# Optimization experiments

Measured on AMD Instinct MI355X. Metric: run time of the kernel, lower is better.

## Reference

```python
import jax, jax.numpy as jnp
import numpy as np

D_IN, D_ATTN, STEPS = 1024, 64, 2
P_TOP, TAU, LN_EPS = 0.9, 1.0, 1e-5
N = 4096

def _xavier(key, shape):
    fan_in, fan_out = shape[0], shape[1]
    lim = jnp.sqrt(6.0 / (fan_in + fan_out))
    return jax.random.uniform(key, shape, jnp.float32, -lim, lim)

def setup_inputs() -> dict:
    key = jax.random.key(0)
    ks = jax.random.split(key, 12)
    X = jax.random.normal(ks[0], (N, D_IN), jnp.float32)
    S = jax.random.uniform(ks[1], (N, N), jnp.float32)
    # weights stored so that y = x @ W (transposed vs torch nn.Linear.weight)
    W1 = _xavier(ks[2], (D_IN, D_ATTN))
    W3 = _xavier(ks[3], (D_IN, D_ATTN))
    W2 = _xavier(ks[4], (D_ATTN, D_ATTN))  # used raw: Q @ W2 @ K.T
    U1_0 = _xavier(ks[5], (D_IN, D_IN))
    U1_1 = _xavier(ks[6], (D_IN, D_IN))
    U2_0 = _xavier(ks[7], (D_IN, D_IN))
    U2_1 = _xavier(ks[8], (D_IN, D_IN))
    gamma = jnp.ones((D_IN,), jnp.float32)
    beta = jnp.zeros((D_IN,), jnp.float32)
    return {"X": X, "S": S, "W1": W1, "W2": W2, "W3": W3,
            "U1_0": U1_0, "U1_1": U1_1, "U2_0": U2_0, "U2_1": U2_1,
            "gamma": gamma, "beta": beta}

def _adj_from_feats(Xa, W1, W2, W3):
    # bilinear attention logits: (N, N)
    Q = Xa @ W1
    K = Xa @ W3
    logits = (Q @ W2) @ K.T / TAU
    n = logits.shape[1]
    order = jnp.argsort(-logits, axis=1)                       # descending
    vals = jnp.take_along_axis(logits, order, axis=1)
    probs = jax.nn.softmax(vals, axis=1)
    csum = jnp.cumsum(probs, axis=1)
    k_i = jnp.sum(csum < P_TOP, axis=1) + 1                    # per-row top-p count
    keep = jnp.arange(n)[None, :] < k_i[:, None]
    masked_sorted = jnp.where(keep, vals, -jnp.inf)
    rows = jnp.arange(n)[:, None]
    masked = jnp.full_like(logits, -jnp.inf).at[rows, order].set(masked_sorted)
    return jax.nn.softmax(masked, axis=1)

def reference(X, S, W1, W2, W3, U1_0, U1_1, U2_0, U2_1, gamma, beta):
    n = X.shape[0]
    S = S + jnp.eye(n, dtype=X.dtype)
    R = S / jnp.clip(S.sum(axis=1, keepdims=True), 1e-12)      # row-normalized prior
    Z = jnp.zeros_like(X)
    Xf, Xa = X, X
    U1s, U2s = (U1_0, U1_1), (U2_0, U2_1)
    for s in range(STEPS):
        A = _adj_from_feats(Xa, W1, W2, W3)
        Xf = R @ Xf
        Xa = A @ Xa
        Z = Z + (Xf @ U1s[s] + Xa @ U2s[s])                    # dropout = identity (eval)
    Y = X + Z
    mu = Y.mean(axis=-1, keepdims=True)
    var = Y.var(axis=-1, keepdims=True)
    return (Y - mu) * jax.lax.rsqrt(var + LN_EPS) * gamma + beta
```

## Files before the change

kernel.cpp:

```cpp
#include <hip/hip_runtime.h>
#include <cstddef>
#include <cmath>

#define N_TOK 4096
#define D_INF 1024
#define OB_Q 384

typedef unsigned long long u64;
typedef __attribute__((ext_vector_type(8))) short bf16x8;
typedef __attribute__((ext_vector_type(4))) float f32x4;

__device__ __forceinline__ float blockSum(float x, float* red) {
#pragma unroll
  for (int o = 32; o; o >>= 1) x += __shfl_xor(x, o);
  __syncthreads();
  if ((threadIdx.x & 63) == 0) red[threadIdx.x >> 6] = x;
  __syncthreads();
  return (red[0] + red[1]) + (red[2] + red[3]);
}

__device__ __forceinline__ int blockSumI512(int x, int* red) {
#pragma unroll
  for (int o = 32; o; o >>= 1) x += __shfl_xor(x, o);
  __syncthreads();
  if ((threadIdx.x & 63) == 0) red[threadIdx.x >> 6] = x;
  __syncthreads();
  int s = 0;
#pragma unroll
  for (int w = 0; w < 8; ++w) s += red[w];
  return s;
}

__device__ __forceinline__ float np_expf(float x) {
  const float log2e = 1.44269504088896341f;
  float q = __builtin_rintf(x * log2e);
  float r = __builtin_fmaf(q, -0.693359375f, x);
  r = __builtin_fmaf(q, 2.12194440e-4f, r);
  float poly = 1.9875691500e-4f;
  poly = __builtin_fmaf(poly, r, 1.3981999507e-3f);
  poly = __builtin_fmaf(poly, r, 8.3334519073e-3f);
  poly = __builtin_fmaf(poly, r, 4.1665795894e-2f);
  poly = __builtin_fmaf(poly, r, 1.6666665459e-1f);
  poly = __builtin_fmaf(poly, r, 5.0000001201e-1f);
  float zz = r * r;
  poly = __builtin_fmaf(poly, zz, r);
  poly = poly + 1.0f;
  return __builtin_ldexpf(poly, (int)q);
}

__device__ __forceinline__ int PIDX(int i) {
  return (i & ~127) | ((i + (i >> 7)) & 127);
}

__device__ float npPairwiseSum4096Rot(const float* __restrict__ buf, float* share) {
  int t = threadIdx.x;
  __syncthreads();
  if (t < 32) {
    const float* a = buf + (t << 7);
    float r0 = a[t & 127], r1 = a[(t + 1) & 127], r2 = a[(t + 2) & 127],
          r3 = a[(t + 3) & 127];
    float r4 = a[(t + 4) & 127], r5 = a[(t + 5) & 127], r6 = a[(t + 6) & 127],
          r7 = a[(t + 7) & 127];
    for (int i = 8; i < 128; i += 8) {
      r0 += a[(i + 0 + t) & 127]; r1 += a[(i + 1 + t) & 127];
      r2 += a[(i + 2 + t) & 127]; r3 += a[(i + 3 + t) & 127];
      r4 += a[(i + 4 + t) & 127]; r5 += a[(i + 5 + t) & 127];
      r6 += a[(i + 6 + t) & 127]; r7 += a[(i + 7 + t) & 127];
    }
    float leaf = ((r0 + r1) + (r2 + r3)) + ((r4 + r5) + (r6 + r7));
    leaf += __shfl_xor(leaf, 1);
    leaf += __shfl_xor(leaf, 2);
    leaf += __shfl_xor(leaf, 4);
    leaf += __shfl_xor(leaf, 8);
    leaf += __shfl_xor(leaf, 16);
    if (t == 0) share[0] = leaf;
  }
  __syncthreads();
  return share[0];
}

__device__ __forceinline__ unsigned desc_key(float v) {
  unsigned u = __float_as_uint(v);
  unsigned m = (u & 0x80000000u) ? ~u : (u | 0x80000000u);
  return ~m;
}
__device__ __forceinline__ float desc_key_inv(unsigned k) {
  unsigned m = ~k;
  return __uint_as_float((m & 0x80000000u) ? (m ^ 0x80000000u) : ~m);
}

__device__ __forceinline__ u64 ballot_match8(int d) {
  u64 m = ~0ull;
#pragma unroll
  for (int b = 0; b < 8; ++b) {
    u64 bal = __ballot((d >> b) & 1);
    m &= ((d >> b) & 1) ? bal : ~bal;
  }
  return m;
}

__device__ __forceinline__ unsigned short f2bf(float f) {
  unsigned u = __float_as_uint(f);
  return (unsigned short)((u + 0x7FFFu + ((u >> 16) & 1u)) >> 16);
}

__global__ __launch_bounds__(256) void rowsum_kernel(const float* __restrict__ S,
                                                     float* __restrict__ rs) {
  __shared__ float red[4];
  const float* s = S + (size_t)blockIdx.x * N_TOK;
  float acc = 0.f;
  for (int j = threadIdx.x; j < N_TOK; j += 256) acc += s[j];
  acc = blockSum(acc, red);
  if (threadIdx.x == 0) rs[blockIdx.x] = 1.0f / fmaxf(acc + 1.0f, 1e-12f);
}

__global__ void wcat_kernel(const float* __restrict__ W1,
                            const float* __restrict__ W3, float* __restrict__ Wc) {
  int r = blockIdx.x;
  int c = threadIdx.x;
  Wc[r * 128 + c] = (c < 64) ? W1[r * 64 + c] : W3[r * 64 + (c - 64)];
}

__global__ __launch_bounds__(256) void qw_kernel(const float* __restrict__ QK,
                                                 const float* __restrict__ W2,
                                                 float* __restrict__ QW) {
  __shared__ float w[64][65];
  int t = threadIdx.x;
#pragma unroll
  for (int v = 0; v < 16; ++v) {
    int idx = t + v * 256;
    w[idx >> 6][idx & 63] = W2[idx];
  }
  __syncthreads();
  int row = blockIdx.x * 4 + (t >> 6);
  int c = t & 63;
  const float* q = QK + (size_t)row * 128;
  float acc = 0.f;
#pragma unroll
  for (int k = 0; k < 64; ++k) acc = __builtin_fmaf(q[k], w[k][c], acc);
  QW[(size_t)row * 64 + c] = acc;
}

__device__ __forceinline__ int ob_step(int rem) {
  if (rem >= 2 * OB_Q) return OB_Q;
  if (rem > OB_Q) return ((rem / 2) + 15) & ~15;
  return rem;
}

template <int BETA>
__global__ __launch_bounds__(256) void gemm_tile(const float* __restrict__ A,
                                                 const float* __restrict__ B,
                                                 float* __restrict__ C,
                                                 int M, int N, int K) {
  __shared__ float As[16][68];
  __shared__ float Bs[16][68];
  int t = threadIdx.x;
  int tx = t & 15, ty = t >> 4;
  int row0 = blockIdx.y * 64, col0 = blockIdx.x * 64;
  float tot[4][4] = {};
  float acc[4][4] = {};
  int next_b = ob_step(K);
  for (int k0 = 0; k0 < K; k0 += 16) {
    if (k0 == next_b) {
#pragma unroll
      for (int i = 0; i < 4; ++i)
#pragma unroll
        for (int j = 0; j < 4; ++j) { tot[i][j] += acc[i][j]; acc[i][j] = 0.f; }
      next_b = k0 + ob_step(K - k0);
    }
#pragma unroll
    for (int v = 0; v < 4; ++v) {
      int idx = t + v * 256;
      int r = idx >> 4, c = idx & 15;
      As[c][r] = A[(size_t)(row0 + r) * K + k0 + c];
    }
#pragma unroll
    for (int v = 0; v < 4; ++v) {
      int idx = t + v * 256;
      int r = idx >> 6, c = idx & 63;
      Bs[r][c] = B[(size_t)(k0 + r) * N + col0 + c];
    }
    __syncthreads();
#pragma unroll
    for (int kk = 0; kk < 16; ++kk) {
      float4 a = *(const float4*)&As[kk][ty * 4];
      float4 b = *(const float4*)&Bs[kk][tx * 4];
      float av[4] = {a.x, a.y, a.z, a.w};
      float bv[4] = {b.x, b.y, b.z, b.w};
#pragma unroll
      for (int i = 0; i < 4; ++i)
#pragma unroll
        for (int j = 0; j < 4; ++j)
          acc[i][j] = __builtin_fmaf(av[i], bv[j], acc[i][j]);
    }
    __syncthreads();
  }
#pragma unroll
  for (int i = 0; i < 4; ++i)
#pragma unroll
    for (int j = 0; j < 4; ++j) tot[i][j] += acc[i][j];
#pragma unroll
  for (int i = 0; i < 4; ++i) {
    float* cp = &C[(size_t)(row0 + ty * 4 + i) * N + col0 + tx * 4];
    float4 o;
    if (BETA) {
      float4 old = *(const float4*)cp;
      o.x = old.x + tot[i][0]; o.y = old.y + tot[i][1];
      o.z = old.z + tot[i][2]; o.w = old.w + tot[i][3];
    } else {
      o.x = tot[i][0]; o.y = tot[i][1]; o.z = tot[i][2]; o.w = tot[i][3];
    }
    *(float4*)cp = o;
  }
}

__global__ __launch_bounds__(256) void spmm_exact(const float* __restrict__ A,
                                                  const float* __restrict__ X,
                                                  float* __restrict__ C) {
  __shared__ unsigned short idxs[N_TOK];
  __shared__ int wq[4];
  int t = threadIdx.x;
  int lane = t & 63, w = t >> 6;
  int row = blockIdx.x;
  const float* a = A + (size_t)row * N_TOK;

  int base = t * 16;
  int c0 = 0;
#pragma unroll
  for (int u = 0; u < 16; ++u) c0 += (a[base + u] != 0.f) ? 1 : 0;
  int incl = c0;
#pragma unroll
  for (int d = 1; d < 64; d <<= 1) {
    int up = __shfl_up(incl, d);
    if (lane >= d) incl += up;
  }
  if (lane == 63) wq[w] = incl;
  __syncthreads();
  int off = 0;
  for (int ww = 0; ww < w; ++ww) off += wq[ww];
  int total = wq[0] + wq[1] + wq[2] + wq[3];
  int pos = off + incl - c0;
#pragma unroll
  for (int u = 0; u < 16; ++u)
    if (a[base + u] != 0.f) idxs[pos++] = (unsigned short)(base + u);
  __syncthreads();

  int c = t * 4;
  float acc0 = 0.f, acc1 = 0.f, acc2 = 0.f, acc3 = 0.f;
  float tt0 = 0.f, tt1 = 0.f, tt2 = 0.f, tt3 = 0.f;
  int nb = ob_step(N_TOK);
  for (int q = 0; q < total; ++q) {
    int j = idxs[q];
    while (j >= nb) {
      tt0 += acc0; tt1 += acc1; tt2 += acc2; tt3 += acc3;
      acc0 = acc1 = acc2 = acc3 = 0.f;
      nb += ob_step(N_TOK - nb);
    }
    float av = a[j];
    float4 xv = *(const float4*)&X[(size_t)j * D_INF + c];
    acc0 = __builtin_fmaf(av, xv.x, acc0);
    acc1 = __builtin_fmaf(av, xv.y, acc1);
    acc2 = __builtin_fmaf(av, xv.z, acc2);
    acc3 = __builtin_fmaf(av, xv.w, acc3);
  }
  tt0 += acc0; tt1 += acc1; tt2 += acc2; tt3 += acc3;
  float4 o = {tt0, tt1, tt2, tt3};
  *(float4*)&C[(size_t)row * D_INF + c] = o;
}

template <int BETA>
__global__ __launch_bounds__(256) void gemm_bf16(const float* __restrict__ A,
                                                 const float* __restrict__ B,
                                                 float* __restrict__ C,
                                                 int M, int N, int K) {
  __shared__ unsigned short As[128 * 32];
  __shared__ unsigned short Bs[128 * 32];
  const int t = threadIdx.x;
  const int l = t & 63, w = t >> 6, wr = w >> 1, wc = w & 1;
  const int m0 = blockIdx.y * 128, n0 = blockIdx.x * 128;

  f32x4 acc[4][4];
#pragma unroll
  for (int i = 0; i < 4; ++i)
#pragma unroll
    for (int j = 0; j < 4; ++j)
#pragma unroll
      for (int r = 0; r < 4; ++r) acc[i][j][r] = 0.f;

  const int argp = t >> 3;
  const int acc4 = (t & 7) * 4;
  const int bkb = t >> 5;
  const int bnb = t & 31;

  for (int k0 = 0; k0 < K; k0 += 32) {
#pragma unroll
    for (int u = 0; u < 4; ++u) {
      int row = argp * 4 + u;
      float4 v = *(const float4*)&A[(size_t)(m0 + row) * K + k0 + acc4];
      ushort4 h;
      h.x = f2bf(v.x); h.y = f2bf(v.y); h.z = f2bf(v.z); h.w = f2bf(v.w);
      int idx = (row * 32 + acc4) ^ (((row >> 1) & 3) << 3);
      *(ushort4*)&As[idx] = h;
    }
    {
      float4 r0 = *(const float4*)&B[(size_t)(k0 + bkb * 4 + 0) * N + n0 + bnb * 4];
      float4 r1 = *(const float4*)&B[(size_t)(k0 + bkb * 4 + 1) * N + n0 + bnb * 4];
      float4 r2 = *(const float4*)&B[(size_t)(k0 + bkb * 4 + 2) * N + n0 + bnb * 4];
      float4 r3 = *(const float4*)&B[(size_t)(k0 + bkb * 4 + 3) * N + n0 + bnb * 4];
      float c0[4] = {r0.x, r0.y, r0.z, r0.w};
      float c1[4] = {r1.x, r1.y, r1.z, r1.w};
      float c2[4] = {r2.x, r2.y, r2.z, r2.w};
      float c3[4] = {r3.x, r3.y, r3.z, r3.w};
#pragma unroll
      for (int u = 0; u < 4; ++u) {
        int nrow = bnb * 4 + u;
        ushort4 h;
        h.x = f2bf(c0[u]); h.y = f2bf(c1[u]); h.z = f2bf(c2[u]); h.w = f2bf(c3[u]);
        int idx = (nrow * 32 + bkb * 4) ^ (((nrow >> 1) & 3) << 3);
        *(ushort4*)&Bs[idx] = h;
      }
    }
    __syncthreads();
    bf16x8 af[4], bfv[4];
    const int kseg = (l >> 4) * 8;
#pragma unroll
    for (int fr = 0; fr < 4; ++fr) {
      int row = wr * 64 + fr * 16 + (l & 15);
      int idx = (row * 32 + kseg) ^ (((row >> 1) & 3) << 3);
      af[fr] = *(const bf16x8*)&As[idx];
    }
#pragma unroll
    for (int fc = 0; fc < 4; ++fc) {
      int nrow = wc * 64 + fc * 16 + (l & 15);
      int idx = (nrow * 32 + kseg) ^ (((nrow >> 1) & 3) << 3);
      bfv[fc] = *(const bf16x8*)&Bs[idx];
    }
#pragma unroll
    for (int fr = 0; fr < 4; ++fr)
#pragma unroll
      for (int fc = 0; fc < 4; ++fc)
        acc[fr][fc] = __builtin_amdgcn_mfma_f32_16x16x32_bf16(af[fr], bfv[fc],
                                                              acc[fr][fc], 0, 0, 0);
    __syncthreads();
  }
#pragma unroll
  for (int fr = 0; fr < 4; ++fr) {
#pragma unroll
    for (int fc = 0; fc < 4; ++fc) {
      int rbase = m0 + wr * 64 + fr * 16 + ((l >> 4) << 2);
      int col = n0 + wc * 64 + fc * 16 + (l & 15);
#pragma unroll
      for (int r = 0; r < 4; ++r) {
        size_t off = (size_t)(rbase + r) * N + col;
        float v = acc[fr][fc][r];
        C[off] = BETA ? (C[off] + v) : v;
      }
    }
  }
}

__global__ __launch_bounds__(256) void logits_abt(const float* __restrict__ QW,
                                                  const float* __restrict__ QK,
                                                  float* __restrict__ L) {
  __shared__ float Aq[64][68];
  __shared__ float Bk[64][68];
  int t = threadIdx.x;
  int tx = t & 15, ty = t >> 4;
  int row0 = blockIdx.y * 64, col0 = blockIdx.x * 64;
#pragma unroll
  for (int v = 0; v < 16; ++v) {
    int idx = t + v * 256;
    int c = idx & 63, r = idx >> 6;
    Aq[c][r] = QW[(size_t)(row0 + r) * 64 + c];
    Bk[c][r] = QK[(size_t)(col0 + r) * 128 + 64 + c];
  }
  __syncthreads();
  float acc[4][4] = {};
#pragma unroll
  for (int c0 = 0; c0 < 64; ++c0) {
    float4 a = *(const float4*)&Aq[c0][ty * 4];
    float4 b = *(const float4*)&Bk[c0][tx * 4];
    float av[4] = {a.x, a.y, a.z, a.w};
    float bv[4] = {b.x, b.y, b.z, b.w};
#pragma unroll
    for (int i = 0; i < 4; ++i)
#pragma unroll
      for (int j = 0; j < 4; ++j)
        acc[i][j] = __builtin_fmaf(av[i], bv[j], acc[i][j]);
  }
#pragma unroll
  for (int i = 0; i < 4; ++i) {
    float4 o = {acc[i][0], acc[i][1], acc[i][2], acc[i][3]};
    *(float4*)&L[(size_t)(row0 + ty * 4 + i) * N_TOK + col0 + tx * 4] = o;
  }
}

__global__ __launch_bounds__(512, 6) void topp_exact(float* __restrict__ L) {
  __shared__ unsigned key[N_TOK];
  __shared__ unsigned scr[N_TOK];
  __shared__ unsigned short hist[8 * 256];
  __shared__ int wred[8];
  __shared__ float fshare;
  __shared__ float mxs;
  __shared__ int kshare;
  __shared__ int ired[8];

  float* l = L + (size_t)blockIdx.x * N_TOK;
  int t = threadIdx.x;
  int lane = t & 63, w = t >> 6;
  u64 below = (lane == 63) ? 0x7FFFFFFFFFFFFFFFull : ((1ull << lane) - 1ull);

  for (int i = t; i < N_TOK; i += 512) key[i] = desc_key(l[i]);
  __syncthreads();

  unsigned* cur = key;
  unsigned* dst = scr;
  for (int pass = 0; pass < 4; ++pass) {
    int s = pass * 8;
    for (int i = t; i < 1024; i += 512) ((int*)hist)[i] = 0;
    __syncthreads();
    unsigned myk[8], mypk[8];
#pragma unroll
    for (int it = 0; it < 8; ++it) {
      unsigned k = cur[w * 512 + it * 64 + lane];
      int d = (k >> s) & 255;
      u64 m = ballot_match8(d);
      int leader = __ffsll(m) - 1;
      int before = (int)__popcll(m & below);
      int old = 0;
      if (lane == leader) {
        old = (int)hist[w * 256 + d];
        hist[w * 256 + d] = (unsigned short)(old + (int)__popcll(m));
      }
      old = __shfl(old, leader);
      myk[it] = k;
      mypk[it] = ((unsigned)(old + before) << 8) | (unsigned)d;
    }
    __syncthreads();
    {
      int li = t * 4;
      int v0 = hist[((li + 0) & 7) * 256 + ((li + 0) >> 3)];
      int v1 = hist[((li + 1) & 7) * 256 + ((li + 1) >> 3)];
      int v2 = hist[((li + 2) & 7) * 256 + ((li + 2) >> 3)];
      int v3 = hist[((li + 3) & 7) * 256 + ((li + 3) >> 3)];
      int sum = v0 + v1 + v2 + v3;
      int incl = sum;
#pragma unroll
      for (int d = 1; d < 64; d <<= 1) {
        int up = __shfl_up(incl, d);
        if (lane >= d) incl += up;
      }
      if (lane == 63) wred[w] = incl;
      __syncthreads();
      int woff = 0;
      for (int ww = 0; ww < w; ++ww) woff += wred[ww];
      int base = woff + incl - sum;
      hist[((li + 0) & 7) * 256 + ((li + 0) >> 3)] = (unsigned short)base;
      hist[((li + 1) & 7) * 256 + ((li + 1) >> 3)] = (unsigned short)(base + v0);
      hist[((li + 2) & 7) * 256 + ((li + 2) >> 3)] = (unsigned short)(base + v0 + v1);
      hist[((li + 3) & 7) * 256 + ((li + 3) >> 3)] =
          (unsigned short)(base + v0 + v1 + v2);
    }
    __syncthreads();
#pragma unroll
    for (int it = 0; it < 8; ++it) {
      int d = mypk[it] & 255;
      int rank = (int)hist[w * 256 + d] + (int)(mypk[it] >> 8);
      dst[rank] = myk[it];
    }
    __syncthreads();
    unsigned* tmp = cur; cur = dst; dst = tmp;
  }

  float* p = (float*)scr;

  if (t == 0) mxs = desc_key_inv(key[0]);
  __syncthreads();
  float mx = mxs;
  for (int i = t; i < N_TOK; i += 512)
    p[PIDX(i)] = np_expf(desc_key_inv(key[i]) - mx);
  float tot = npPairwiseSum4096Rot(p, &fshare);

  for (int i = t; i < N_TOK; i += 512) p[PIDX(i)] = p[PIDX(i)] / tot;
  __syncthreads();

  if (t == 0) {
    float c = 0.f;
    int cnt2 = 0;
    for (int j = 0; j < N_TOK; ++j) {
      c += p[PIDX(j)];
      if (c < 0.9f) ++cnt2; else break;
    }
    kshare = (cnt2 + 1 < N_TOK) ? cnt2 + 1 : N_TOK;
  }
  __syncthreads();
  int kcut = kshare;

  unsigned kt = key[kcut - 1];
  int cg = 0, ce = 0;
  for (int i = t; i < N_TOK; i += 512) {
    unsigned kv = key[i];
    cg += (kv < kt) ? 1 : 0;
    ce += (kv == kt) ? 1 : 0;
  }
  cg = blockSumI512(cg, ired);
  ce = blockSumI512(ce, ired);
  int m_keep = kcut - cg;
  bool allties = (m_keep == ce);
  __syncthreads();

  float* sbuf = (float*)scr;

  for (int i = t; i < N_TOK; i += 512) {
    float v = l[i];
    unsigned vk = desc_key(v);
    key[i] = __float_as_uint(v);
    bool keep = allties ? (vk <= kt) : (vk < kt);
    sbuf[PIDX(i)] = keep ? np_expf(v - mx) : 0.f;
  }
  __syncthreads();
  if (!allties && t == 0) {
    int taken = 0;
    for (int i = 0; i < N_TOK && taken < m_keep; ++i) {
      float v = __uint_as_float(key[i]);
      if (desc_key(v) == kt) { sbuf[PIDX(i)] = np_expf(v - mx); ++taken; }
    }
  }
  float denom = npPairwiseSum4096Rot(sbuf, &fshare);

  for (int i = t; i < N_TOK; i += 512) l[i] = sbuf[PIDX(i)] / denom;
}

__global__ __launch_bounds__(256) void xf_update(float* __restrict__ Xf,
                                                 const float* __restrict__ T,
                                                 const float* __restrict__ rs) {
  int idx = blockIdx.x * 256 + threadIdx.x;
  int row = idx >> 8;
  float r = rs[row];
  float4 a = ((const float4*)T)[idx];
  float4 b = ((const float4*)Xf)[idx];
  float4 o;
  o.x = (a.x + b.x) * r; o.y = (a.y + b.y) * r;
  o.z = (a.z + b.z) * r; o.w = (a.w + b.w) * r;
  ((float4*)Xf)[idx] = o;
}

__global__ __launch_bounds__(256) void ln_kernel(const float* __restrict__ X,
                                                 float* __restrict__ out,
                                                 const float* __restrict__ gamma,
                                                 const float* __restrict__ beta) {
  __shared__ float red[4];
  size_t base = (size_t)blockIdx.x * D_INF;
  int t = threadIdx.x;
  float y[4];
  float s = 0.f, ss = 0.f;
#pragma unroll
  for (int i = 0; i < 4; ++i) {
    int c = i * 256 + t;
    y[i] = X[base + c] + out[base + c];
    s += y[i];
    ss += y[i] * y[i];
  }
  s = blockSum(s, red);
  ss = blockSum(ss, red);
  float mean = s * (1.f / 1024.f);
  float var = ss * (1.f / 1024.f) - mean * mean;
  float rstd = rsqrtf(var + 1e-5f);
#pragma unroll
  for (int i = 0; i < 4; ++i) {
    int c = i * 256 + t;
    out[base + c] = (y[i] - mean) * rstd * gamma[c] + beta[c];
  }
}

extern "C" void kernel_launch(void* const* d_in, const int* in_sizes, int n_in,
                              void* d_out, int out_size, void* d_ws, size_t ws_size,
                              hipStream_t stream) {
  const float* X    = (const float*)d_in[0];
  const float* S    = (const float*)d_in[1];
  const float* W1   = (const float*)d_in[2];
  const float* W2   = (const float*)d_in[3];
  const float* W3   = (const float*)d_in[4];
  const float* U1_0 = (const float*)d_in[5];
  const float* U1_1 = (const float*)d_in[6];
  const float* U2_0 = (const float*)d_in[7];
  const float* U2_1 = (const float*)d_in[8];
  const float* gamma = (const float*)d_in[9];
  const float* beta  = (const float*)d_in[10];
  float* Z = (float*)d_out;

  const size_t ND = (size_t)N_TOK * D_INF;
  const size_t NN = (size_t)N_TOK * N_TOK;
  float* Xf  = (float*)d_ws;
  float* Xa0 = Xf  + ND;
  float* Xa1 = Xa0 + ND;
  float* T   = Xa1 + ND;
  float* L   = T   + ND;
  float* QKb = L   + NN;
  float* QWb = QKb + (size_t)N_TOK * 128;
  float* Wc  = QWb + (size_t)N_TOK * 64;
  float* rs  = Wc  + (size_t)D_INF * 128;

  hipMemcpyAsync(Xf, X, ND * sizeof(float), hipMemcpyDeviceToDevice, stream);
  rowsum_kernel<<<N_TOK, 256, 0, stream>>>(S, rs);
  wcat_kernel<<<D_INF, 128, 0, stream>>>(W1, W3, Wc);

  dim3 g128(D_INF / 128, N_TOK / 128);

  gemm_tile<0><<<dim3(2, 64), 256, 0, stream>>>(X, Wc, QKb, N_TOK, 128, D_INF);
  qw_kernel<<<N_TOK / 4, 256, 0, stream>>>(QKb, W2, QWb);
  logits_abt<<<dim3(64, 64), 256, 0, stream>>>(QWb, QKb, L);
  topp_exact<<<N_TOK, 512, 0, stream>>>(L);
  gemm_bf16<0><<<g128, 256, 0, stream>>>(S, Xf, T, N_TOK, D_INF, N_TOK);
  xf_update<<<4096, 256, 0, stream>>>(Xf, T, rs);
  spmm_exact<<<N_TOK, 256, 0, stream>>>(L, X, Xa0);
  gemm_bf16<0><<<g128, 256, 0, stream>>>(Xf, U1_0, Z, N_TOK, D_INF, D_INF);
  gemm_bf16<1><<<g128, 256, 0, stream>>>(Xa0, U2_0, Z, N_TOK, D_INF, D_INF);

  gemm_tile<0><<<dim3(2, 64), 256, 0, stream>>>(Xa0, Wc, QKb, N_TOK, 128, D_INF);
  qw_kernel<<<N_TOK / 4, 256, 0, stream>>>(QKb, W2, QWb);
  logits_abt<<<dim3(64, 64), 256, 0, stream>>>(QWb, QKb, L);
  topp_exact<<<N_TOK, 512, 0, stream>>>(L);
  gemm_bf16<0><<<g128, 256, 0, stream>>>(S, Xf, T, N_TOK, D_INF, N_TOK);
  xf_update<<<4096, 256, 0, stream>>>(Xf, T, rs);
  gemm_bf16<0><<<g128, 256, 0, stream>>>(L, Xa0, Xa1, N_TOK, D_INF, N_TOK);
  gemm_bf16<1><<<g128, 256, 0, stream>>>(Xf, U1_1, Z, N_TOK, D_INF, D_INF);
  gemm_bf16<1><<<g128, 256, 0, stream>>>(Xa1, U2_1, Z, N_TOK, D_INF, D_INF);

  ln_kernel<<<N_TOK, 256, 0, stream>>>(X, Z, gamma, beta);
}
```

Measured before the change: 1.939 ms.

## Co-schedule independent GEMMs with top-p and QK projection in fused multi-role kernels

Independent stages are merged into combined launches that dispatch on block index. The QK projection runs alongside the S@Xf prior GEMM, the top-p rows alongside the Xf@U1 or S@Xf GEMM, and the second QK projection alongside Xa0@U2_0. The xf_update elementwise pass and the initial Xf copy are removed by folding (T+Xf)*rs into the GEMM epilogue, which writes to ping-pong Xf buffers. This is meant to fill idle CUs and cut launch and memory traffic, but it adds a 512-thread GEMM variant with smaller per-wave tiles and shared-memory sizing constraints that can hurt occupancy.

```diff
diff --git a/kernel.cpp b/kernel.cpp
--- a/kernel.cpp
+++ b/kernel.cpp
@@ -5,6 +5,10 @@
 #define N_TOK 4096
 #define D_INF 1024
 #define OB_Q 384
+
+#define MODE_STORE 0
+#define MODE_ACCUM 1
+#define MODE_XF 2
 
 typedef unsigned long long u64;
 typedef __attribute__((ext_vector_type(8))) short bf16x8;
@@ -104,6 +108,12 @@
   return (unsigned short)((u + 0x7FFFu + ((u >> 16) & 1u)) >> 16);
 }
 
+__device__ __forceinline__ int ob_step(int rem) {
+  if (rem >= 2 * OB_Q) return OB_Q;
+  if (rem > OB_Q) return ((rem / 2) + 15) & ~15;
+  return rem;
+}
+
 __global__ __launch_bounds__(256) void rowsum_kernel(const float* __restrict__ S,
                                                      float* __restrict__ rs) {
   __shared__ float red[4];
@@ -141,76 +151,39 @@
   QW[(size_t)row * 64 + c] = acc;
 }
 
-__device__ __forceinline__ int ob_step(int rem) {
-  if (rem >= 2 * OB_Q) return OB_Q;
-  if (rem > OB_Q) return ((rem / 2) + 15) & ~15;
-  return rem;
-}
-
-template <int BETA>
-__global__ __launch_bounds__(256) void gemm_tile(const float* __restrict__ A,
-                                                 const float* __restrict__ B,
-                                                 float* __restrict__ C,
-                                                 int M, int N, int K) {
-  __shared__ float As[16][68];
-  __shared__ float Bs[16][68];
+__global__ __launch_bounds__(256) void logits_abt(const float* __restrict__ QW,
+                                                  const float* __restrict__ QK,
+                                                  float* __restrict__ L) {
+  __shared__ float Aq[64][68];
+  __shared__ float Bk[64][68];
   int t = threadIdx.x;
   int tx = t & 15, ty = t >> 4;
   int row0 = blockIdx.y * 64, col0 = blockIdx.x * 64;
-  float tot[4][4] = {};
+#pragma unroll
+  for (int v = 0; v < 16; ++v) {
+    int idx = t + v * 256;
+    int c = idx & 63, r = idx >> 6;
+    Aq[c][r] = QW[(size_t)(row0 + r) * 64 + c];
+    Bk[c][r] = QK[(size_t)(col0 + r) * 128 + 64 + c];
+  }
+  __syncthreads();
   float acc[4][4] = {};
-  int next_b = ob_step(K);
-  for (int k0 = 0; k0 < K; k0 += 16) {
-    if (k0 == next_b) {
-#pragma unroll
-      for (int i = 0; i < 4; ++i)
-#pragma unroll
-        for (int j = 0; j < 4; ++j) { tot[i][j] += acc[i][j]; acc[i][j] = 0.f; }
-      next_b = k0 + ob_step(K - k0);
-    }
-#pragma unroll
-    for (int v = 0; v < 4; ++v) {
-      int idx = t + v * 256;
-      int r = idx >> 4, c = idx & 15;
-      As[c][r] = A[(size_t)(row0 + r) * K + k0 + c];
-    }
-#pragma unroll
-    for (int v = 0; v < 4; ++v) {
-      int idx = t + v * 256;
-      int r = idx >> 6, c = idx & 63;
-      Bs[r][c] = B[(size_t)(k0 + r) * N + col0 + c];
-    }
-    __syncthreads();
-#pragma unroll
-    for (int kk = 0; kk < 16; ++kk) {
-      float4 a = *(const float4*)&As[kk][ty * 4];
-      float4 b = *(const float4*)&Bs[kk][tx * 4];
-      float av[4] = {a.x, a.y, a.z, a.w};
-      float bv[4] = {b.x, b.y, b.z, b.w};
-#pragma unroll
-      for (int i = 0; i < 4; ++i)
-#pragma unroll
-        for (int j = 0; j < 4; ++j)
-          acc[i][j] = __builtin_fmaf(av[i], bv[j], acc[i][j]);
-    }
-    __syncthreads();
-  }
-#pragma unroll
-  for (int i = 0; i < 4; ++i)
-#pragma unroll
-    for (int j = 0; j < 4; ++j) tot[i][j] += acc[i][j];
+#pragma unroll
+  for (int c0 = 0; c0 < 64; ++c0) {
+    float4 a = *(const float4*)&Aq[c0][ty * 4];
+    float4 b = *(const float4*)&Bk[c0][tx * 4];
+    float av[4] = {a.x, a.y, a.z, a.w};
+    float bv[4] = {b.x, b.y, b.z, b.w};
+#pragma unroll
+    for (int i = 0; i < 4; ++i)
+#pragma unroll
+      for (int j = 0; j < 4; ++j)
+        acc[i][j] = __builtin_fmaf(av[i], bv[j], acc[i][j]);
+  }
 #pragma unroll
   for (int i = 0; i < 4; ++i) {
-    float* cp = &C[(size_t)(row0 + ty * 4 + i) * N + col0 + tx * 4];
-    float4 o;
-    if (BETA) {
-      float4 old = *(const float4*)cp;
-      o.x = old.x + tot[i][0]; o.y = old.y + tot[i][1];
-      o.z = old.z + tot[i][2]; o.w = old.w + tot[i][3];
-    } else {
-      o.x = tot[i][0]; o.y = tot[i][1]; o.z = tot[i][2]; o.w = tot[i][3];
-    }
-    *(float4*)cp = o;
+    float4 o = {acc[i][0], acc[i][1], acc[i][2], acc[i][3]};
+    *(float4*)&L[(size_t)(row0 + ty * 4 + i) * N_TOK + col0 + tx * 4] = o;
   }
 }
 
@@ -268,16 +241,76 @@
   *(float4*)&C[(size_t)row * D_INF + c] = o;
 }
 
-template <int BETA>
-__global__ __launch_bounds__(256) void gemm_bf16(const float* __restrict__ A,
-                                                 const float* __restrict__ B,
-                                                 float* __restrict__ C,
-                                                 int M, int N, int K) {
-  __shared__ unsigned short As[128 * 32];
-  __shared__ unsigned short Bs[128 * 32];
+__device__ void gemm_tile_body(const float* __restrict__ A,
+                               const float* __restrict__ B,
+                               float* __restrict__ C,
+                               int N, int K, int bx, int by, char* raw) {
+  float* As = (float*)raw;
+  float* Bs = As + 16 * 68;
+  int t = threadIdx.x;
+  int tx = t & 15, ty = t >> 4;
+  int row0 = by * 64, col0 = bx * 64;
+  float tot[4][4] = {};
+  float acc[4][4] = {};
+  int next_b = ob_step(K);
+  for (int k0 = 0; k0 < K; k0 += 16) {
+    if (k0 == next_b) {
+#pragma unroll
+      for (int i = 0; i < 4; ++i)
+#pragma unroll
+        for (int j = 0; j < 4; ++j) { tot[i][j] += acc[i][j]; acc[i][j] = 0.f; }
+      next_b = k0 + ob_step(K - k0);
+    }
+#pragma unroll
+    for (int v = 0; v < 4; ++v) {
+      int idx = t + v * 256;
+      int r = idx >> 4, c = idx & 15;
+      As[c * 68 + r] = A[(size_t)(row0 + r) * K + k0 + c];
+    }
+#pragma unroll
+    for (int v = 0; v < 4; ++v) {
+      int idx = t + v * 256;
+      int r = idx >> 6, c = idx & 63;
+      Bs[r * 68 + c] = B[(size_t)(k0 + r) * N + col0 + c];
+    }
+    __syncthreads();
+#pragma unroll
+    for (int kk = 0; kk < 16; ++kk) {
+      float4 a = *(const float4*)&As[kk * 68 + ty * 4];
+      float4 b = *(const float4*)&Bs[kk * 68 + tx * 4];
+      float av[4] = {a.x, a.y, a.z, a.w};
+      float bv[4] = {b.x, b.y, b.z, b.w};
+#pragma unroll
+      for (int i = 0; i < 4; ++i)
+#pragma unroll
+        for (int j = 0; j < 4; ++j)
+          acc[i][j] = __builtin_fmaf(av[i], bv[j], acc[i][j]);
+    }
+    __syncthreads();
+  }
+#pragma unroll
+  for (int i = 0; i < 4; ++i)
+#pragma unroll
+    for (int j = 0; j < 4; ++j) tot[i][j] += acc[i][j];
+#pragma unroll
+  for (int i = 0; i < 4; ++i) {
+    float4 o = {tot[i][0], tot[i][1], tot[i][2], tot[i][3]};
+    *(float4*)&C[(size_t)(row0 + ty * 4 + i) * N + col0 + tx * 4] = o;
+  }
+}
+
+__device__ void gemm_bf16_body256(const float* __restrict__ A,
+                                  const float* __restrict__ B,
+                                  float* __restrict__ C,
+                                  int N, int K, int mode,
+                                  const float* __restrict__ xfold,
+                                  const float* __restrict__ rs,
+                                  int bx, int by, char* raw) {
+  unsigned short* As = (unsigned short*)raw;
+  unsigned short* Bs = As + 4096;
   const int t = threadIdx.x;
   const int l = t & 63, w = t >> 6, wr = w >> 1, wc = w & 1;
-  const int m0 = blockIdx.y * 128, n0 = blockIdx.x * 128;
+  const int m0 = by * 128, n0 = bx * 128;
 
   f32x4 acc[4][4];
 #pragma unroll
@@ -351,64 +384,125 @@
       int col = n0 + wc * 64 + fc * 16 + (l & 15);
 #pragma unroll
       for (int r = 0; r < 4; ++r) {
-        size_t off = (size_t)(rbase + r) * N + col;
+        int row = rbase + r;
+        size_t off = (size_t)row * N + col;
         float v = acc[fr][fc][r];
-        C[off] = BETA ? (C[off] + v) : v;
+        if (mode == MODE_STORE) C[off] = v;
+        else if (mode == MODE_ACCUM) C[off] = C[off] + v;
+        else { float sum = v + xfold[off]; C[off] = sum * rs[row]; }
       }
     }
   }
 }
 
-__global__ __launch_bounds__(256) void logits_abt(const float* __restrict__ QW,
-                                                  const float* __restrict__ QK,
-                                                  float* __restrict__ L) {
-  __shared__ float Aq[64][68];
-  __shared__ float Bk[64][68];
-  int t = threadIdx.x;
-  int tx = t & 15, ty = t >> 4;
-  int row0 = blockIdx.y * 64, col0 = blockIdx.x * 64;
-#pragma unroll
-  for (int v = 0; v < 16; ++v) {
-    int idx = t + v * 256;
-    int c = idx & 63, r = idx >> 6;
-    Aq[c][r] = QW[(size_t)(row0 + r) * 64 + c];
-    Bk[c][r] = QK[(size_t)(col0 + r) * 128 + 64 + c];
-  }
-  __syncthreads();
-  float acc[4][4] = {};
-#pragma unroll
-  for (int c0 = 0; c0 < 64; ++c0) {
-    float4 a = *(const float4*)&Aq[c0][ty * 4];
-    float4 b = *(const float4*)&Bk[c0][tx * 4];
-    float av[4] = {a.x, a.y, a.z, a.w};
-    float bv[4] = {b.x, b.y, b.z, b.w};
-#pragma unroll
-    for (int i = 0; i < 4; ++i)
-#pragma unroll
-      for (int j = 0; j < 4; ++j)
-        acc[i][j] = __builtin_fmaf(av[i], bv[j], acc[i][j]);
-  }
-#pragma unroll
-  for (int i = 0; i < 4; ++i) {
-    float4 o = {acc[i][0], acc[i][1], acc[i][2], acc[i][3]};
-    *(float4*)&L[(size_t)(row0 + ty * 4 + i) * N_TOK + col0 + tx * 4] = o;
-  }
-}
-
-__global__ __launch_bounds__(512, 6) void topp_exact(float* __restrict__ L) {
-  __shared__ unsigned key[N_TOK];
-  __shared__ unsigned scr[N_TOK];
-  __shared__ unsigned short hist[8 * 256];
-  __shared__ int wred[8];
-  __shared__ float fshare;
-  __shared__ float mxs;
-  __shared__ int kshare;
-  __shared__ int ired[8];
-
-  float* l = L + (size_t)blockIdx.x * N_TOK;
+__device__ void gemm_bf16_body512(const float* __restrict__ A,
+                                  const float* __restrict__ B,
+                                  float* __restrict__ C,
+                                  int N, int K, int mode,
+                                  const float* __restrict__ xfold,
+                                  const float* __restrict__ rs,
+                                  int bx, int by, char* raw) {
+  unsigned short* As = (unsigned short*)raw;
+  unsigned short* Bs = As + 4096;
+  const int t = threadIdx.x;
+  const int l = t & 63, w = t >> 6;
+  const int wr = w >> 2, wc = w & 3;
+  const int m0 = by * 128, n0 = bx * 128;
+
+  f32x4 acc[4][2];
+#pragma unroll
+  for (int i = 0; i < 4; ++i)
+#pragma unroll
+    for (int j = 0; j < 2; ++j)
+#pragma unroll
+      for (int r = 0; r < 4; ++r) acc[i][j][r] = 0.f;
+
+  const int arow = t >> 2;
+  const int ak = (t & 3) * 8;
+  const int bkb = (t >> 5) * 2;
+  const int bnb = (t & 31) * 4;
+
+  for (int k0 = 0; k0 < K; k0 += 32) {
+    {
+      float4 v0 = *(const float4*)&A[(size_t)(m0 + arow) * K + k0 + ak];
+      float4 v1 = *(const float4*)&A[(size_t)(m0 + arow) * K + k0 + ak + 4];
+      ushort4 h0, h1;
+      h0.x = f2bf(v0.x); h0.y = f2bf(v0.y); h0.z = f2bf(v0.z); h0.w = f2bf(v0.w);
+      h1.x = f2bf(v1.x); h1.y = f2bf(v1.y); h1.z = f2bf(v1.z); h1.w = f2bf(v1.w);
+      int idx = (arow * 32 + ak) ^ (((arow >> 1) & 3) << 3);
+      *(ushort4*)&As[idx] = h0;
+      *(ushort4*)&As[idx + 4] = h1;
+    }
+    {
+      float4 r0 = *(const float4*)&B[(size_t)(k0 + bkb + 0) * N + n0 + bnb];
+      float4 r1 = *(const float4*)&B[(size_t)(k0 + bkb + 1) * N + n0 + bnb];
+      float c0[4] = {r0.x, r0.y, r0.z, r0.w};
+      float c1[4] = {r1.x, r1.y, r1.z, r1.w};
+#pragma unroll
+      for (int u = 0; u < 4; ++u) {
+        int nrow = bnb + u;
+        ushort2 h;
+        h.x = f2bf(c0[u]); h.y = f2bf(c1[u]);
+        int idx = (nrow * 32 + bkb) ^ (((nrow >> 1) & 3) << 3);
+        *(ushort2*)&Bs[idx] = h;
+      }
+    }
+    __syncthreads();
+    bf16x8 af[4], bfv[2];
+    const int kseg = (l >> 4) * 8;
+#pragma unroll
+    for (int fr = 0; fr < 4; ++fr) {
+      int row = wr * 64 + fr * 16 + (l & 15);
+      int idx = (row * 32 + kseg) ^ (((row >> 1) & 3) << 3);
+      af[fr] = *(const bf16x8*)&As[idx];
+    }
+#pragma unroll
+    for (int fc = 0; fc < 2; ++fc) {
+      int nrow = wc * 32 + fc * 16 + (l & 15);
+      int idx = (nrow * 32 + kseg) ^ (((nrow >> 1) & 3) << 3);
+      bfv[fc] = *(const bf16x8*)&Bs[idx];
+    }
+#pragma unroll
+    for (int fr = 0; fr < 4; ++fr)
+#pragma unroll
+      for (int fc = 0; fc < 2; ++fc)
+        acc[fr][fc] = __builtin_amdgcn_mfma_f32_16x16x32_bf16(af[fr], bfv[fc],
+                                                              acc[fr][fc], 0, 0, 0);
+    __syncthreads();
+  }
+#pragma unroll
+  for (int fr = 0; fr < 4; ++fr) {
+#pragma unroll
+    for (int fc = 0; fc < 2; ++fc) {
+      int rbase = m0 + wr * 64 + fr * 16 + ((l >> 4) << 2);
+      int col = n0 + wc * 32 + fc * 16 + (l & 15);
+#pragma unroll
+      for (int r = 0; r < 4; ++r) {
+        int row = rbase + r;
+        size_t off = (size_t)row * N + col;
+        float v = acc[fr][fc][r];
+        if (mode == MODE_STORE) C[off] = v;
+        else if (mode == MODE_ACCUM) C[off] = C[off] + v;
+        else { float sum = v + xfold[off]; C[off] = sum * rs[row]; }
+      }
+    }
+  }
+}
+
+__device__ void topp_body(float* __restrict__ l, char* raw) {
+  unsigned* key = (unsigned*)raw;
+  unsigned* scr = key + 4096;
+  unsigned short* hist = (unsigned short*)(scr + 4096);
+  int* wred = (int*)(raw + 36864);
+  float* fshare = (float*)(raw + 36896);
+  float* mxs = (float*)(raw + 36900);
+  int* kshare = (int*)(raw + 36904);
+  int* ired = (int*)(raw + 36908);
+
   int t = threadIdx.x;
   int lane = t & 63, w = t >> 6;
-  u64 below = (lane == 63) ? 0x7FFFFFFFFFFFFFFFull : ((1ull << lane) - 1ull);
+  u64 below = (1ull << lane) - 1ull;
+  if (lane == 63) below = 0x7FFFFFFFFFFFFFFFull;
 
   for (int i = t; i < N_TOK; i += 512) key[i] = desc_key(l[i]);
   __syncthreads();
@@ -421,19 +515,19 @@
     __syncthreads();
     unsigned myk[8], mypk[8];
 #pragma unroll
+    for (int it = 0; it < 8; ++it) myk[it] = cur[w * 512 + it * 64 + lane];
+#pragma unroll
     for (int it = 0; it < 8; ++it) {
-      unsigned k = cur[w * 512 + it * 64 + lane];
-      int d = (k >> s) & 255;
+      int d = (myk[it] >> s) & 255;
       u64 m = ballot_match8(d);
+      int before = (int)__popcll(m & below);
       int leader = __ffsll(m) - 1;
-      int before = (int)__popcll(m & below);
       int old = 0;
-      if (lane == leader) {
+      if (before == 0) {
         old = (int)hist[w * 256 + d];
         hist[w * 256 + d] = (unsigned short)(old + (int)__popcll(m));
       }
       old = __shfl(old, leader);
-      myk[it] = k;
       mypk[it] = ((unsigned)(old + before) << 8) | (unsigned)d;
     }
     __syncthreads();
@@ -474,12 +568,12 @@
 
   float* p = (float*)scr;
 
-  if (t == 0) mxs = desc_key_inv(key[0]);
-  __syncthreads();
-  float mx = mxs;
+  if (t == 0) mxs[0] = desc_key_inv(key[0]);
+  __syncthreads();
+  float mx = mxs[0];
   for (int i = t; i < N_TOK; i += 512)
     p[PIDX(i)] = np_expf(desc_key_inv(key[i]) - mx);
-  float tot = npPairwiseSum4096Rot(p, &fshare);
+  float tot = npPairwiseSum4096Rot(p, fshare);
 
   for (int i = t; i < N_TOK; i += 512) p[PIDX(i)] = p[PIDX(i)] / tot;
   __syncthreads();
@@ -491,10 +585,10 @@
       c += p[PIDX(j)];
       if (c < 0.9f) ++cnt2; else break;
     }
-    kshare = (cnt2 + 1 < N_TOK) ? cnt2 + 1 : N_TOK;
-  }
-  __syncthreads();
-  int kcut = kshare;
+    kshare[0] = (cnt2 + 1 < N_TOK) ? cnt2 + 1 : N_TOK;
+  }
+  __syncthreads();
+  int kcut = kshare[0];
 
   unsigned kt = key[kcut - 1];
   int cg = 0, ce = 0;
@@ -526,23 +620,45 @@
       if (desc_key(v) == kt) { sbuf[PIDX(i)] = np_expf(v - mx); ++taken; }
     }
   }
-  float denom = npPairwiseSum4096Rot(sbuf, &fshare);
+  float denom = npPairwiseSum4096Rot(sbuf, fshare);
 
   for (int i = t; i < N_TOK; i += 512) l[i] = sbuf[PIDX(i)] / denom;
 }
 
-__global__ __launch_bounds__(256) void xf_update(float* __restrict__ Xf,
-                                                 const float* __restrict__ T,
-                                                 const float* __restrict__ rs) {
-  int idx = blockIdx.x * 256 + threadIdx.x;
-  int row = idx >> 8;
-  float r = rs[row];
-  float4 a = ((const float4*)T)[idx];
-  float4 b = ((const float4*)Xf)[idx];
-  float4 o;
-  o.x = (a.x + b.x) * r; o.y = (a.y + b.y) * r;
-  o.z = (a.z + b.z) * r; o.w = (a.w + b.w) * r;
-  ((float4*)Xf)[idx] = o;
+__global__ __launch_bounds__(256, 4) void fat256(
+    int nexact, const float* Ae, const float* Be, float* Ce, int Ne, int Ke,
+    const float* Ab, const float* Bb, float* Cb, int Nb, int Kb, int mode,
+    const float* xfold, const float* rs) {
+  __shared__ __align__(16) char raw[16384];
+  int bid = blockIdx.x;
+  if (bid < nexact) {
+    int xt = Ne >> 6;
+    gemm_tile_body(Ae, Be, Ce, Ne, Ke, bid % xt, bid / xt, raw);
+  } else {
+    int b2 = bid - nexact;
+    int xt = Nb >> 7;
+    gemm_bf16_body256(Ab, Bb, Cb, Nb, Kb, mode, xfold, rs, b2 % xt, b2 / xt, raw);
+  }
+}
+
+__global__ __launch_bounds__(512, 8) void fat512(
+    int ngemm, const float* Ab, const float* Bb, float* Cb, int Nb, int Kb,
+    int mode, const float* xfold, const float* rs, float* L) {
+  __shared__ __align__(16) char raw[37120];
+  int bid = blockIdx.x;
+  if (bid < ngemm) {
+    int xt = Nb >> 7;
+    gemm_bf16_body512(Ab, Bb, Cb, Nb, Kb, mode, xfold, rs, bid % xt, bid / xt, raw);
+  } else {
+    topp_body(L + (size_t)(bid - ngemm) * N_TOK, raw);
+  }
+}
+
+__global__ __launch_bounds__(256, 4) void gemm_bf16k(const float* A, const float* B,
+                                                     float* C, int N, int K, int mode) {
+  __shared__ __align__(16) char raw[16384];
+  gemm_bf16_body256(A, B, C, N, K, mode, nullptr, nullptr,
+                    blockIdx.x, blockIdx.y, raw);
 }
 
 __global__ __launch_bounds__(256) void ln_kernel(const float* __restrict__ X,
@@ -591,41 +707,39 @@
 
   const size_t ND = (size_t)N_TOK * D_INF;
   const size_t NN = (size_t)N_TOK * N_TOK;
-  float* Xf  = (float*)d_ws;
-  float* Xa0 = Xf  + ND;
+  float* Xf0 = (float*)d_ws;
+  float* Xf1 = Xf0 + ND;
+  float* Xa0 = Xf1 + ND;
   float* Xa1 = Xa0 + ND;
-  float* T   = Xa1 + ND;
-  float* L   = T   + ND;
+  float* L   = Xa1 + ND;
   float* QKb = L   + NN;
   float* QWb = QKb + (size_t)N_TOK * 128;
   float* Wc  = QWb + (size_t)N_TOK * 64;
   float* rs  = Wc  + (size_t)D_INF * 128;
 
-  hipMemcpyAsync(Xf, X, ND * sizeof(float), hipMemcpyDeviceToDevice, stream);
   rowsum_kernel<<<N_TOK, 256, 0, stream>>>(S, rs);
   wcat_kernel<<<D_INF, 128, 0, stream>>>(W1, W3, Wc);
 
   dim3 g128(D_INF / 128, N_TOK / 128);
 
-  gemm_tile<0><<<dim3(2, 64), 256, 0, stream>>>(X, Wc, QKb, N_TOK, 128, D_INF);
+  fat256<<<384, 256, 0, stream>>>(128, X, Wc, QKb, 128, D_INF,
+                                  S, X, Xf1, D_INF, N_TOK, MODE_XF, X, rs);
   qw_kernel<<<N_TOK / 4, 256, 0, stream>>>(QKb, W2, QWb);
   logits_abt<<<dim3(64, 64), 256, 0, stream>>>(QWb, QKb, L);
-  topp_exact<<<N_TOK, 512, 0, stream>>>(L);
-  gemm_bf16<0><<<g128, 256, 0, stream>>>(S, Xf, T, N_TOK, D_INF, N_TOK);
-  xf_update<<<4096, 256, 0, stream>>>(Xf, T, rs);
+  fat512<<<4352, 512, 0, stream>>>(256, Xf1, U1_0, Z, D_INF, D_INF,
+                                   MODE_STORE, nullptr, nullptr, L);
   spmm_exact<<<N_TOK, 256, 0, stream>>>(L, X, Xa0);
-  gemm_bf16<0><<<g128, 256, 0, stream>>>(Xf, U1_0, Z, N_TOK, D_INF, D_INF);
-  gemm_bf16<1><<<g128, 256, 0, stream>>>(Xa0, U2_0, Z, N_TOK, D_INF, D_INF);
-
-  gemm_tile<0><<<dim3(2, 64), 256, 0, stream>>>(Xa0, Wc, QKb, N_TOK, 128, D_INF);
+  fat256<<<384, 256, 0, stream>>>(128, Xa0, Wc, QKb, 128, D_INF,
+                                  Xa0, U2_0, Z, D_INF, D_INF, MODE_ACCUM,
+                                  nullptr, nullptr);
+
   qw_kernel<<<N_TOK / 4, 256, 0, stream>>>(QKb, W2, QWb);
   logits_abt<<<dim3(64, 64), 256, 0, stream>>>(QWb, QKb, L);
-  topp_exact<<<N_TOK, 512, 0, stream>>>(L);
-  gemm_bf16<0><<<g128, 256, 0, stream>>>(S, Xf, T, N_TOK, D_INF, N_TOK);
-  xf_update<<<4096, 256, 0, stream>>>(Xf, T, rs);
-  gemm_bf16<0><<<g128, 256, 0, stream>>>(L, Xa0, Xa1, N_TOK, D_INF, N_TOK);
-  gemm_bf16<1><<<g128, 256, 0, stream>>>(Xf, U1_1, Z, N_TOK, D_INF, D_INF);
-  gemm_bf16<1><<<g128, 256, 0, stream>>>(Xa1, U2_1, Z, N_TOK, D_INF, D_INF);
+  fat512<<<4352, 512, 0, stream>>>(256, S, Xf1, Xf0, D_INF, N_TOK,
+                                   MODE_XF, Xf1, rs, L);
+  gemm_bf16k<<<g128, 256, 0, stream>>>(Xf0, U1_1, Z, D_INF, D_INF, MODE_ACCUM);
+  gemm_bf16k<<<g128, 256, 0, stream>>>(L, Xa0, Xa1, D_INF, N_TOK, MODE_STORE);
+  gemm_bf16k<<<g128, 256, 0, stream>>>(Xa1, U2_1, Z, D_INF, D_INF, MODE_ACCUM);
 
   ln_kernel<<<N_TOK, 256, 0, stream>>>(X, Z, gamma, beta);
 }
```

Result: slower. 2.090 ms (+7.8%).

## Fuse Xf update into GEMM epilogue and co-launch independent bf16 GEMMs

Applied to the files above, without the earlier changes.

Folds the xf_update elementwise pass into the S@Xf bf16 GEMM epilogue (adds the old Xf and scales by the row reciprocal), which removes the temporary T buffer, the extra kernel and the initial Xf memcpy by ping-ponging Xf0/Xf1. It also merges the independent Xf@U1_1 and L@Xa0 GEMMs into one 512-block launch so they can fill the GPU together. It adds launch_bounds occupancy hints and small radix-sort ballot tweaks in topp_exact. The fused launch mixes K=1024 and K=4096 tiles, so load balance may be uneven.

```diff
diff --git a/kernel.cpp b/kernel.cpp
--- a/kernel.cpp
+++ b/kernel.cpp
@@ -5,6 +5,10 @@
 #define N_TOK 4096
 #define D_INF 1024
 #define OB_Q 384
+
+#define MODE_STORE 0
+#define MODE_ACCUM 1
+#define MODE_XF 2
 
 typedef unsigned long long u64;
 typedef __attribute__((ext_vector_type(8))) short bf16x8;
@@ -104,6 +108,12 @@
   return (unsigned short)((u + 0x7FFFu + ((u >> 16) & 1u)) >> 16);
 }
 
+__device__ __forceinline__ int ob_step(int rem) {
+  if (rem >= 2 * OB_Q) return OB_Q;
+  if (rem > OB_Q) return ((rem / 2) + 15) & ~15;
+  return rem;
+}
+
 __global__ __launch_bounds__(256) void rowsum_kernel(const float* __restrict__ S,
                                                      float* __restrict__ rs) {
   __shared__ float red[4];
@@ -141,13 +151,42 @@
   QW[(size_t)row * 64 + c] = acc;
 }
 
-__device__ __forceinline__ int ob_step(int rem) {
-  if (rem >= 2 * OB_Q) return OB_Q;
-  if (rem > OB_Q) return ((rem / 2) + 15) & ~15;
-  return rem;
-}
-
-template <int BETA>
+__global__ __launch_bounds__(256) void logits_abt(const float* __restrict__ QW,
+                                                  const float* __restrict__ QK,
+                                                  float* __restrict__ L) {
+  __shared__ float Aq[64][68];
+  __shared__ float Bk[64][68];
+  int t = threadIdx.x;
+  int tx = t & 15, ty = t >> 4;
+  int row0 = blockIdx.y * 64, col0 = blockIdx.x * 64;
+#pragma unroll
+  for (int v = 0; v < 16; ++v) {
+    int idx = t + v * 256;
+    int c = idx & 63, r = idx >> 6;
+    Aq[c][r] = QW[(size_t)(row0 + r) * 64 + c];
+    Bk[c][r] = QK[(size_t)(col0 + r) * 128 + 64 + c];
+  }
+  __syncthreads();
+  float acc[4][4] = {};
+#pragma unroll
+  for (int c0 = 0; c0 < 64; ++c0) {
+    float4 a = *(const float4*)&Aq[c0][ty * 4];
+    float4 b = *(const float4*)&Bk[c0][tx * 4];
+    float av[4] = {a.x, a.y, a.z, a.w};
+    float bv[4] = {b.x, b.y, b.z, b.w};
+#pragma unroll
+    for (int i = 0; i < 4; ++i)
+#pragma unroll
+      for (int j = 0; j < 4; ++j)
+        acc[i][j] = __builtin_fmaf(av[i], bv[j], acc[i][j]);
+  }
+#pragma unroll
+  for (int i = 0; i < 4; ++i) {
+    float4 o = {acc[i][0], acc[i][1], acc[i][2], acc[i][3]};
+    *(float4*)&L[(size_t)(row0 + ty * 4 + i) * N_TOK + col0 + tx * 4] = o;
+  }
+}
+
 __global__ __launch_bounds__(256) void gemm_tile(const float* __restrict__ A,
                                                  const float* __restrict__ B,
                                                  float* __restrict__ C,
@@ -201,16 +240,8 @@
     for (int j = 0; j < 4; ++j) tot[i][j] += acc[i][j];
 #pragma unroll
   for (int i = 0; i < 4; ++i) {
-    float* cp = &C[(size_t)(row0 + ty * 4 + i) * N + col0 + tx * 4];
-    float4 o;
-    if (BETA) {
-      float4 old = *(const float4*)cp;
-      o.x = old.x + tot[i][0]; o.y = old.y + tot[i][1];
-      o.z = old.z + tot[i][2]; o.w = old.w + tot[i][3];
-    } else {
-      o.x = tot[i][0]; o.y = tot[i][1]; o.z = tot[i][2]; o.w = tot[i][3];
-    }
-    *(float4*)cp = o;
+    float4 o = {tot[i][0], tot[i][1], tot[i][2], tot[i][3]};
+    *(float4*)&C[(size_t)(row0 + ty * 4 + i) * N + col0 + tx * 4] = o;
   }
 }
 
@@ -268,16 +299,19 @@
   *(float4*)&C[(size_t)row * D_INF + c] = o;
 }
 
-template <int BETA>
-__global__ __launch_bounds__(256) void gemm_bf16(const float* __restrict__ A,
-                                                 const float* __restrict__ B,
-                                                 float* __restrict__ C,
-                                                 int M, int N, int K) {
+template <int MODE>
+__device__ void gemm_bf16_body(const float* __restrict__ A,
+                               const float* __restrict__ B,
+                               float* __restrict__ C,
+                               int N, int K,
+                               const float* __restrict__ xfold,
+                               const float* __restrict__ rs,
+                               int bx, int by) {
   __shared__ unsigned short As[128 * 32];
   __shared__ unsigned short Bs[128 * 32];
   const int t = threadIdx.x;
   const int l = t & 63, w = t >> 6, wr = w >> 1, wc = w & 1;
-  const int m0 = blockIdx.y * 128, n0 = blockIdx.x * 128;
+  const int m0 = by * 128, n0 = bx * 128;
 
   f32x4 acc[4][4];
 #pragma unroll
@@ -351,47 +385,38 @@
       int col = n0 + wc * 64 + fc * 16 + (l & 15);
 #pragma unroll
       for (int r = 0; r < 4; ++r) {
-        size_t off = (size_t)(rbase + r) * N + col;
+        int row = rbase + r;
+        size_t off = (size_t)row * N + col;
         float v = acc[fr][fc][r];
-        C[off] = BETA ? (C[off] + v) : v;
+        if (MODE == MODE_STORE) C[off] = v;
+        else if (MODE == MODE_ACCUM) C[off] = C[off] + v;
+        else { float sum = v + xfold[off]; C[off] = sum * rs[row]; }
       }
     }
   }
 }
 
-__global__ __launch_bounds__(256) void logits_abt(const float* __restrict__ QW,
-                                                  const float* __restrict__ QK,
-                                                  float* __restrict__ L) {
-  __shared__ float Aq[64][68];
-  __shared__ float Bk[64][68];
-  int t = threadIdx.x;
-  int tx = t & 15, ty = t >> 4;
-  int row0 = blockIdx.y * 64, col0 = blockIdx.x * 64;
-#pragma unroll
-  for (int v = 0; v < 16; ++v) {
-    int idx = t + v * 256;
-    int c = idx & 63, r = idx >> 6;
-    Aq[c][r] = QW[(size_t)(row0 + r) * 64 + c];
-    Bk[c][r] = QK[(size_t)(col0 + r) * 128 + 64 + c];
-  }
-  __syncthreads();
-  float acc[4][4] = {};
-#pragma unroll
-  for (int c0 = 0; c0 < 64; ++c0) {
-    float4 a = *(const float4*)&Aq[c0][ty * 4];
-    float4 b = *(const float4*)&Bk[c0][tx * 4];
-    float av[4] = {a.x, a.y, a.z, a.w};
-    float bv[4] = {b.x, b.y, b.z, b.w};
-#pragma unroll
-    for (int i = 0; i < 4; ++i)
-#pragma unroll
-      for (int j = 0; j < 4; ++j)
-        acc[i][j] = __builtin_fmaf(av[i], bv[j], acc[i][j]);
-  }
-#pragma unroll
-  for (int i = 0; i < 4; ++i) {
-    float4 o = {acc[i][0], acc[i][1], acc[i][2], acc[i][3]};
-    *(float4*)&L[(size_t)(row0 + ty * 4 + i) * N_TOK + col0 + tx * 4] = o;
+template <int MODE>
+__global__ __launch_bounds__(256, 4) void gemm_bf16(const float* A, const float* B,
+                                                    float* C, int N, int K,
+                                                    const float* xfold,
+                                                    const float* rs) {
+  gemm_bf16_body<MODE>(A, B, C, N, K, xfold, rs, blockIdx.x, blockIdx.y);
+}
+
+__global__ __launch_bounds__(256, 4) void fat2bf16(
+    int n0, const float* A0, const float* B0, float* C0, int N0, int K0,
+    const float* A1, const float* B1, float* C1, int N1, int K1) {
+  int bid = blockIdx.x;
+  if (bid < n0) {
+    int xt = N0 >> 7;
+    gemm_bf16_body<MODE_ACCUM>(A0, B0, C0, N0, K0, nullptr, nullptr,
+                               bid % xt, bid / xt);
+  } else {
+    int b2 = bid - n0;
+    int xt = N1 >> 7;
+    gemm_bf16_body<MODE_STORE>(A1, B1, C1, N1, K1, nullptr, nullptr,
+                               b2 % xt, b2 / xt);
   }
 }
 
@@ -408,7 +433,8 @@
   float* l = L + (size_t)blockIdx.x * N_TOK;
   int t = threadIdx.x;
   int lane = t & 63, w = t >> 6;
-  u64 below = (lane == 63) ? 0x7FFFFFFFFFFFFFFFull : ((1ull << lane) - 1ull);
+  u64 below = (1ull << lane) - 1ull;
+  if (lane == 63) below = 0x7FFFFFFFFFFFFFFFull;
 
   for (int i = t; i < N_TOK; i += 512) key[i] = desc_key(l[i]);
   __syncthreads();
@@ -421,19 +447,19 @@
     __syncthreads();
     unsigned myk[8], mypk[8];
 #pragma unroll
+    for (int it = 0; it < 8; ++it) myk[it] = cur[w * 512 + it * 64 + lane];
+#pragma unroll
     for (int it = 0; it < 8; ++it) {
-      unsigned k = cur[w * 512 + it * 64 + lane];
-      int d = (k >> s) & 255;
+      int d = (myk[it] >> s) & 255;
       u64 m = ballot_match8(d);
+      int before = (int)__popcll(m & below);
       int leader = __ffsll(m) - 1;
-      int before = (int)__popcll(m & below);
       int old = 0;
-      if (lane == leader) {
+      if (before == 0) {
         old = (int)hist[w * 256 + d];
         hist[w * 256 + d] = (unsigned short)(old + (int)__popcll(m));
       }
       old = __shfl(old, leader);
-      myk[it] = k;
       mypk[it] = ((unsigned)(old + before) << 8) | (unsigned)d;
     }
     __syncthreads();
@@ -529,20 +555,6 @@
   float denom = npPairwiseSum4096Rot(sbuf, &fshare);
 
   for (int i = t; i < N_TOK; i += 512) l[i] = sbuf[PIDX(i)] / denom;
-}
-
-__global__ __launch_bounds__(256) void xf_update(float* __restrict__ Xf,
-                                                 const float* __restrict__ T,
-                                                 const float* __restrict__ rs) {
-  int idx = blockIdx.x * 256 + threadIdx.x;
-  int row = idx >> 8;
-  float r = rs[row];
-  float4 a = ((const float4*)T)[idx];
-  float4 b = ((const float4*)Xf)[idx];
-  float4 o;
-  o.x = (a.x + b.x) * r; o.y = (a.y + b.y) * r;
-  o.z = (a.z + b.z) * r; o.w = (a.w + b.w) * r;
-  ((float4*)Xf)[idx] = o;
 }
 
 __global__ __launch_bounds__(256) void ln_kernel(const float* __restrict__ X,
@@ -591,41 +603,41 @@
 
   const size_t ND = (size_t)N_TOK * D_INF;
   const size_t NN = (size_t)N_TOK * N_TOK;
-  float* Xf  = (float*)d_ws;
-  float* Xa0 = Xf  + ND;
+  float* Xf0 = (float*)d_ws;
+  float* Xf1 = Xf0 + ND;
+  float* Xa0 = Xf1 + ND;
   float* Xa1 = Xa0 + ND;
-  float* T   = Xa1 + ND;
-  float* L   = T   + ND;
+  float* L   = Xa1 + ND;
   float* QKb = L   + NN;
   float* QWb = QKb + (size_t)N_TOK * 128;
   float* Wc  = QWb + (size_t)N_TOK * 64;
   float* rs  = Wc  + (size_t)D_INF * 128;
 
-  hipMemcpyAsync(Xf, X, ND * sizeof(float), hipMemcpyDeviceToDevice, stream);
   rowsum_kernel<<<N_TOK, 256, 0, stream>>>(S, rs);
   wcat_kernel<<<D_INF, 128, 0, stream>>>(W1, W3, Wc);
 
   dim3 g128(D_INF / 128, N_TOK / 128);
 
-  gemm_tile<0><<<dim3(2, 64), 256, 0, stream>>>(X, Wc, QKb, N_TOK, 128, D_INF);
+  gemm_tile<<<dim3(2, 64), 256, 0, stream>>>(X, Wc, QKb, N_TOK, 128, D_INF);
   qw_kernel<<<N_TOK / 4, 256, 0, stream>>>(QKb, W2, QWb);
   logits_abt<<<dim3(64, 64), 256, 0, stream>>>(QWb, QKb, L);
   topp_exact<<<N_TOK, 512, 0, stream>>>(L);
-  gemm_bf16<0><<<g128, 256, 0, stream>>>(S, Xf, T, N_TOK, D_INF, N_TOK);
-  xf_update<<<4096, 256, 0, stream>>>(Xf, T, rs);
+  gemm_bf16<MODE_XF><<<g128, 256, 0, stream>>>(S, X, Xf1, D_INF, N_TOK, X, rs);
   spmm_exact<<<N_TOK, 256, 0, stream>>>(L, X, Xa0);
-  gemm_bf16<0><<<g128, 256, 0, stream>>>(Xf, U1_0, Z, N_TOK, D_INF, D_INF);
-  gemm_bf16<1><<<g128, 256, 0, stream>>>(Xa0, U2_0, Z, N_TOK, D_INF, D_INF);
-
-  gemm_tile<0><<<dim3(2, 64), 256, 0, stream>>>(Xa0, Wc, QKb, N_TOK, 128, D_INF);
+  gemm_bf16<MODE_STORE><<<g128, 256, 0, stream>>>(Xf1, U1_0, Z, D_INF, D_INF,
+                                                  nullptr, nullptr);
+  gemm_bf16<MODE_ACCUM><<<g128, 256, 0, stream>>>(Xa0, U2_0, Z, D_INF, D_INF,
+                                                  nullptr, nullptr);
+
+  gemm_tile<<<dim3(2, 64), 256, 0, stream>>>(Xa0, Wc, QKb, N_TOK, 128, D_INF);
   qw_kernel<<<N_TOK / 4, 256, 0, stream>>>(QKb, W2, QWb);
   logits_abt<<<dim3(64, 64), 256, 0, stream>>>(QWb, QKb, L);
   topp_exact<<<N_TOK, 512, 0, stream>>>(L);
-  gemm_bf16<0><<<g128, 256, 0, stream>>>(S, Xf, T, N_TOK, D_INF, N_TOK);
-  xf_update<<<4096, 256, 0, stream>>>(Xf, T, rs);
-  gemm_bf16<0><<<g128, 256, 0, stream>>>(L, Xa0, Xa1, N_TOK, D_INF, N_TOK);
-  gemm_bf16<1><<<g128, 256, 0, stream>>>(Xf, U1_1, Z, N_TOK, D_INF, D_INF);
-  gemm_bf16<1><<<g128, 256, 0, stream>>>(Xa1, U2_1, Z, N_TOK, D_INF, D_INF);
+  gemm_bf16<MODE_XF><<<g128, 256, 0, stream>>>(S, Xf1, Xf0, D_INF, N_TOK, Xf1, rs);
+  fat2bf16<<<512, 256, 0, stream>>>(256, Xf0, U1_1, Z, D_INF, D_INF,
+                                    L, Xa0, Xa1, D_INF, N_TOK);
+  gemm_bf16<MODE_ACCUM><<<g128, 256, 0, stream>>>(Xa1, U2_1, Z, D_INF, D_INF,
+                                                  nullptr, nullptr);
 
   ln_kernel<<<N_TOK, 256, 0, stream>>>(X, Z, gamma, beta);
 }
```

Measured after the change: 2.123 ms. 9.5% more time.
